# Optimization experiments

Measured on AMD Instinct MI355X. Metric: run time of the kernel, lower is better.

Reference implementation:

```python
import jax, jax.numpy as jnp
import numpy as np

H = 128   # d_model / features
N = 32    # kept complex modes (d_state=64 -> 32 conjugate pairs)
B = 8
L = 8192


def setup_inputs() -> dict:
    key = jax.random.key(0)
    ks = jax.random.split(key, 8)
    x = jax.random.normal(ks[0], (B, H, L), jnp.float32)
    # S4D (diagonal SSM) kernel parameters; channels=2 for bidirectional
    C_re = (jax.random.normal(ks[1], (2, H, N), jnp.float32) * (0.5 ** 0.5))
    C_im = (jax.random.normal(ks[2], (2, H, N), jnp.float32) * (0.5 ** 0.5))
    log_A_real = jnp.log(0.5 * jnp.ones((H, N), jnp.float32))          # S4D-Lin init
    A_imag = jnp.tile(np.pi * jnp.arange(N, dtype=jnp.float32), (H, 1))
    # log_dt uniform in [log(1e-3), log(1e-1)]
    u = jax.random.uniform(ks[3], (H,), jnp.float32)
    log_dt = u * (np.log(0.1) - np.log(0.001)) + np.log(0.001)
    D = jax.random.normal(ks[4], (H,), jnp.float32)                    # skip term
    W_pw = jax.random.normal(ks[5], (H, H), jnp.float32) / np.sqrt(H)  # 1x1 conv weight (out, in)
    gamma = jnp.ones((H,), jnp.float32)
    beta = jnp.zeros((H,), jnp.float32)
    return {"x": x, "C_re": C_re, "C_im": C_im, "log_A_real": log_A_real,
            "A_imag": A_imag, "log_dt": log_dt, "D": D, "W_pw": W_pw,
            "gamma": gamma, "beta": beta}


def reference(x, C_re, C_im, log_A_real, A_imag, log_dt, D, W_pw, gamma, beta):
    Lx = x.shape[-1]
    # ---- S4D SSM kernel via Vandermonde (ZOH discretization) ----
    A = -jnp.exp(log_A_real) + 1j * A_imag                 # (H, N) complex
    dt = jnp.exp(log_dt)[:, None]                          # (H, 1)
    dtA = A * dt                                           # (H, N)
    C = C_re + 1j * C_im                                   # (2, H, N)
    Kc = C * ((jnp.exp(dtA) - 1.0) / A)                    # (2, H, N)
    vand = jnp.exp(dtA[:, :, None] * jnp.arange(Lx))       # (H, N, L)
    k = 2.0 * jnp.einsum('chn,hnl->chl', Kc, vand).real    # (2, H, L)
    # ---- bidirectional: causal half + anticausal (flipped) half ----
    k_full = (jnp.pad(k[0], ((0, 0), (0, Lx)))
              + jnp.pad(k[1][:, ::-1], ((0, 0), (Lx, 0))))  # (H, 2L)
    # ---- FFT convolution ----
    n = 2 * Lx
    y = jnp.fft.irfft(jnp.fft.rfft(x, n=n) * jnp.fft.rfft(k_full, n=n), n=n)[..., :Lx]
    y = y + x * D[:, None]                                 # skip connection
    y = jax.nn.gelu(y, approximate=False)                  # FFTConv default activation
    # ---- pointwise 1x1 conv (no bias) ----
    y = jnp.einsum('bhl,oh->bol', y, W_pw)
    # ---- BatchNorm1d (training-mode batch statistics) ----
    mean = jnp.mean(y, axis=(0, 2), keepdims=True)
    var = jnp.var(y, axis=(0, 2), keepdims=True)
    y = (y - mean) * jax.lax.rsqrt(var + 1e-5) * gamma[:, None] + beta[:, None]
    # ---- ELU + residual (dropout p=0) ----
    return jax.nn.elu(y) + x
```

## Files before the change

kernel.cpp:

```cpp
#include <hip/hip_runtime.h>
#include <math.h>

#define HCH   128
#define NMODE 32
#define BB    8
#define LLEN  8192
#define LC    256
#define CCH   (LLEN / LC)
#define ROWS  (BB * HCH)

typedef unsigned int uint;
typedef _Float16 f16x8 __attribute__((ext_vector_type(8)));
typedef float    f32x4 __attribute__((ext_vector_type(4)));

static __device__ __forceinline__ uint pk2(float a, float b) {
    union { _Float16 h[2]; uint u; } v;
    v.h[0] = (_Float16)a; v.h[1] = (_Float16)b;
    return v.u;
}

__device__ __forceinline__ float gelu_f(float y) {
    float z = fabsf(y) * 0.7071067811865476f;
    float p = fmaf(z, 0.078108f, 0.000972f);
    p = fmaf(z, p, 0.230389f);
    p = fmaf(z, p, 0.278393f);
    p = fmaf(z, p, 1.0f);
    float p2 = p * p;
    float p4 = p2 * p2;
    float er = 1.f - __builtin_amdgcn_rcpf(p4);
    float s  = copysignf(er, y);
    return 0.5f * y * (1.f + s);
}

#define DPP_ADD(v, ctrl) { int _t = __builtin_amdgcn_update_dpp(0, __float_as_int(v), \
                             (ctrl), 0xF, 0xF, true); (v) += __int_as_float(_t); }

__global__ __launch_bounds__(256) void k_prep(const float* __restrict__ C_re,
                                              const float* __restrict__ C_im,
                                              const float* __restrict__ logA,
                                              const float* __restrict__ Aim,
                                              const float* __restrict__ logdt,
                                              const float* __restrict__ W,
                                              _Float16* __restrict__ aT,
                                              _Float16* __restrict__ eT,
                                              _Float16* __restrict__ Wh,
                                              float* __restrict__ Pw,
                                              float* __restrict__ stats) {
    __shared__ float2 PL[32 * 257];
    __shared__ float4 G01[32];
    __shared__ float4 HG[32];
    __shared__ float2 WL[32];
    __shared__ float k0L[256], k1L[256];
    int tid  = threadIdx.x;
    int h    = blockIdx.x >> 1;
    int half = blockIdx.x & 1;
    if (blockIdx.x == 0) stats[tid] = 0.f;
    if (half == 0 && tid < 128) Wh[h * 128 + tid] = (_Float16)W[h * 128 + tid];
    if (tid < 32) {
        int n = tid, idx = h * 32 + n;
        float ar = expf(logA[idx]);
        float ai = Aim[idx];
        float dt = expf(logdt[h]);
        float dre = -ar * dt, dim = ai * dt;
        float er = expf(dre);
        float wr = er * cosf(dim), wi = er * sinf(dim);
        WL[n] = (float2){wr, wi};
        if (half == 0) {
            float eL = expf(dre * 256.f);
            Pw[idx]        = eL * cosf(dim * 256.f);
            Pw[4096 + idx] = eL * sinf(dim * 256.f);
        }
        float den  = ar * ar + ai * ai;
        float numr = -(wr - 1.f) * ar + wi * ai;
        float numi = -wi * ar - (wr - 1.f) * ai;
        float Kr = numr / den, Ki = numi / den;
        float c0r = C_re[idx],        c0i = C_im[idx];
        float c1r = C_re[4096 + idx], c1i = C_im[4096 + idx];
        float g0r = 2.f * (c0r * Kr - c0i * Ki), g0i = 2.f * (c0r * Ki + c0i * Kr);
        float g1r = 2.f * (c1r * Kr - c1i * Ki);
        float g1i = 2.f * (c1r * Ki + c1i * Kr);
        G01[n] = (float4){g0r, g0i, g1r, g1i};
        HG[n]  = (float4){g0r * wr - g0i * wi, g0r * wi + g0i * wr, g1r, g1i};
    }
    __syncthreads();
    {
        int n = tid & 31, tg = tid >> 5;
        float2 w = WL[n];
        float w2r = w.x * w.x - w.y * w.y,   w2i = 2.f * w.x * w.y;
        float w4r = w2r * w2r - w2i * w2i,   w4i = 2.f * w2r * w2i;
        float w8r = w4r * w4r - w4i * w4i,   w8i = 2.f * w4r * w4i;
        float pr = (tg & 1) ? w.x : 1.f;
        float pi = (tg & 1) ? w.y : 0.f;
        if (tg & 2) { float t2 = pr * w2r - pi * w2i; pi = pr * w2i + pi * w2r; pr = t2; }
        if (tg & 4) { float t4 = pr * w4r - pi * w4i; pi = pr * w4i + pi * w4r; pr = t4; }
        float2* row = &PL[n * 257];
        #pragma unroll
        for (int j = 0; j < 32; j++) {
            row[tg + 8 * j] = (float2){pr, pi};
            float tr = pr * w8r - pi * w8i; pi = pr * w8i + pi * w8r; pr = tr;
        }
    }
    __syncthreads();
    {
        int tau = tid;
        float s0 = 0.f, s1 = 0.f;
        #pragma unroll
        for (int n = 0; n < 32; n++) {
            float2 p = PL[n * 257 + tau];
            float4 g = G01[n];
            s0 += g.x * p.x - g.y * p.y;
            s1 += g.z * p.x - g.w * p.y;
        }
        k0L[tau] = s0; k1L[tau] = s1;
    }
    __syncthreads();
    #pragma unroll 4
    for (int i = 0; i < 64; i++) {
        int idx = i * 256 + tid;
        int t  = half * 128 + (idx >> 7);
        int sp = (idx & 127) << 1;
        float v0 = (sp     <= t) ? k0L[t - sp]     : k1L[sp - t - 1];
        float v1 = (sp + 1 <= t) ? k0L[t - sp - 1] : k1L[sp - t];
        *(uint*)&aT[((size_t)(h * 256 + t)) * 384 + sp] = pk2(v0, v1);
    }
    #pragma unroll 4
    for (int i = 0; i < 16; i++) {
        int idx = i * 256 + tid;
        int n = idx & 31;
        int t = half * 128 + (idx >> 5);
        float2 pt = PL[n * 257 + t];
        float2 pu = PL[n * 257 + 255 - t];
        float4 hg = HG[n];
        size_t rb = ((size_t)(h * 256 + t)) * 384;
        *(uint*)&aT[rb + 256 + 2 * n] = pk2(hg.x * pt.x - hg.y * pt.y,
                                            -(hg.x * pt.y + hg.y * pt.x));
        *(uint*)&aT[rb + 320 + 2 * n] = pk2(hg.z * pu.x - hg.w * pu.y,
                                            -(hg.z * pu.y + hg.w * pu.x));
    }
    #pragma unroll 4
    for (int i = 0; i < 16; i++) {
        int idx = i * 256 + tid;
        int n = idx >> 7;
        int s = half * 128 + (idx & 127);
        float2 ps = PL[n * 257 + s];
        float2 pu = PL[n * 257 + 255 - s];
        size_t base = (size_t)h * 128 * 256;
        eT[base + (size_t)(2 * n) * 256 + s]      = (_Float16)pu.x;
        eT[base + (size_t)(2 * n + 1) * 256 + s]  = (_Float16)pu.y;
        eT[base + (size_t)(64 + 2 * n) * 256 + s] = (_Float16)ps.x;
        eT[base + (size_t)(65 + 2 * n) * 256 + s] = (_Float16)ps.y;
    }
}

__global__ __launch_bounds__(256, 2) void k_states_g(const float* __restrict__ x,
                                                     const _Float16* __restrict__ eT,
                                                     float* __restrict__ S_end,
                                                     _Float16* __restrict__ xh) {
    __shared__ _Float16 At[2][128 * 40];
    __shared__ _Float16 Bt[2][128 * 40];
    int tid = threadIdx.x;
    int xcd = blockIdx.x & 7, slot = blockIdx.x >> 3;
    int h = xcd * 16 + (slot >> 1), mt = slot & 1;
    int wave = tid >> 6, lane = tid & 63;
    int wm = wave >> 1, wn = wave & 1;
    int lrow = lane & 15, quad = lane >> 4;
    int koff = quad * 8;
    f32x4 acc[4][4];
    #pragma unroll
    for (int a = 0; a < 4; a++)
        #pragma unroll
        for (int b = 0; b < 4; b++) acc[a][b] = (f32x4){0.f, 0.f, 0.f, 0.f};

    const int chA = tid >> 3, segA = tid & 7;
    const size_t xbase = (((size_t)(mt * 4) * HCH + h) << 13) + (chA << 8) + segA * 4;
    const int rB = tid >> 2, sgB = tid & 3;

    float4 ar[4]; uint4 br[2];
    #define LOADA_S(kk) { _Pragma("unroll") for (int i = 0; i < 4; i++) \
        ar[i] = *(const float4*)(x + xbase + ((size_t)i << 20) + (kk)); }
    #define LOADB_S(kk) { _Pragma("unroll") for (int i = 0; i < 2; i++) \
        br[i] = *(const uint4*)(eT + ((size_t)(h * 128 + rB + 64 * i)) * 256 + (kk) + sgB * 8); }
    #define WRITE_S(buf, kk) { _Pragma("unroll") for (int i = 0; i < 4; i++) { \
            uint2 o; o.x = pk2(ar[i].x, ar[i].y); o.y = pk2(ar[i].z, ar[i].w); \
            *(uint2*)&At[buf][(chA + 32 * i) * 40 + segA * 4] = o; \
            *(uint2*)&xh[xbase + ((size_t)i << 20) + (kk)] = o; } \
        _Pragma("unroll") for (int i = 0; i < 2; i++) \
            *(uint4*)&Bt[buf][(rB + 64 * i) * 40 + sgB * 8] = br[i]; }

    LOADA_S(0); LOADB_S(0);
    WRITE_S(0, 0);
    __syncthreads();
    for (int kt = 0; kt < 8; kt++) {
        int cur = kt & 1;
        if (kt < 7) { LOADA_S((kt + 1) * 32); LOADB_S((kt + 1) * 32); }
        f16x8 a[4], b[4];
        #pragma unroll
        for (int f = 0; f < 4; f++) {
            a[f] = *(const f16x8*)&At[cur][(wm * 64 + f * 16 + lrow) * 40 + koff];
            b[f] = *(const f16x8*)&Bt[cur][(wn * 64 + f * 16 + lrow) * 40 + koff];
        }
        #pragma unroll
        for (int fi = 0; fi < 4; fi++)
            #pragma unroll
            for (int fj = 0; fj < 4; fj++)
                acc[fi][fj] = __builtin_amdgcn_mfma_f32_16x16x32_f16(a[fi], b[fj], acc[fi][fj], 0, 0, 0);
        if (kt < 7) {
            WRITE_S(cur ^ 1, (kt + 1) * 32);
            __syncthreads();
        }
    }
    #pragma unroll
    for (int fi = 0; fi < 4; fi++) {
        #pragma unroll
        for (int fj = 0; fj < 4; fj++) {
            int srow = wn * 64 + fj * 16 + lrow;
            #pragma unroll
            for (int rg = 0; rg < 4; rg++) {
                int bc = mt * 128 + wm * 64 + fi * 16 + quad * 4 + rg;
                S_end[((size_t)(h * 256 + bc)) * 128 + srow] = acc[fi][fj][rg];
            }
        }
    }
    #undef LOADA_S
    #undef LOADB_S
    #undef WRITE_S
}

__global__ void k_carries(const float* __restrict__ S_end, const float* __restrict__ Pw,
                          _Float16* __restrict__ carr) {
    int i = blockIdx.x * 256 + threadIdx.x;
    int n = i & 31; int d = (i >> 5) & 1; int row = i >> 6;
    int h = row & (HCH - 1), b = row >> 7;
    int pi = h * NMODE + n;
    float wLr = Pw[pi], wLi = Pw[4096 + pi];
    int srow = d * 64 + 2 * n;
    float cr = 0.f, ci = 0.f;
    if (d == 0) {
        for (int c = 0; c < CCH; c++) {
            size_t base = ((size_t)(h * 256 + b * 32 + c)) * 128 + srow;
            carr[base] = (_Float16)cr; carr[base + 1] = (_Float16)ci;
            float sr = S_end[base], si = S_end[base + 1];
            float nr = fmaf(wLr, cr, -wLi * ci) + sr;
            float ni = fmaf(wLi, cr,  wLr * ci) + si;
            cr = nr; ci = ni;
        }
    } else {
        for (int c = CCH - 1; c >= 0; c--) {
            size_t base = ((size_t)(h * 256 + b * 32 + c)) * 128 + srow;
            carr[base] = (_Float16)cr; carr[base + 1] = (_Float16)ci;
            float sr = S_end[base], si = S_end[base + 1];
            float nr = fmaf(wLr, cr, -wLi * ci) + sr;
            float ni = fmaf(wLi, cr,  wLr * ci) + si;
            cr = nr; ci = ni;
        }
    }
}

__global__ __launch_bounds__(256, 2) void k_conv_g(const _Float16* __restrict__ xh,
                                                   const _Float16* __restrict__ aT,
                                                   const _Float16* __restrict__ carr,
                                                   const float* __restrict__ D,
                                                   _Float16* __restrict__ Yg) {
    __shared__ _Float16 At[2][128 * 40];
    __shared__ _Float16 Bt[2][128 * 40];
    int tid = threadIdx.x;
    int xcd = blockIdx.x & 7, slot = blockIdx.x >> 3;
    int p = xcd * 32 + (slot >> 1);
    int mt = slot & 1;
    int h = p >> 1, nt = p & 1;
    int wave = tid >> 6, lane = tid & 63;
    int wm = wave >> 1, wn = wave & 1;
    int lrow = lane & 15, quad = lane >> 4;
    int koff = quad * 8;
    f32x4 acc[4][4];
    #pragma unroll
    for (int a = 0; a < 4; a++)
        #pragma unroll
        for (int b = 0; b < 4; b++) acc[a][b] = (f32x4){0.f, 0.f, 0.f, 0.f};

    const int rS = tid >> 2, sgS = tid & 3;

    uint4 a_r[2], b_r[2];
    #define LOADA_C(kk) { _Pragma("unroll") for (int i = 0; i < 2; i++) { \
            int bc = mt * 128 + rS + 64 * i; \
            a_r[i] = ((kk) < 256) \
              ? *(const uint4*)(xh + (((size_t)((bc >> 5) * HCH + h)) << 13) + ((bc & 31) << 8) + (kk) + sgS * 8) \
              : *(const uint4*)(carr + ((size_t)(h * 256 + bc)) * 128 + ((kk) - 256) + sgS * 8); } }
    #define LOADB_C(kk) { _Pragma("unroll") for (int i = 0; i < 2; i++) \
        b_r[i] = *(const uint4*)(aT + ((size_t)(h * 256 + nt * 128 + rS + 64 * i)) * 384 + (kk) + sgS * 8); }
    #define WRITE_C(buf) { _Pragma("unroll") for (int i = 0; i < 2; i++) { \
            *(uint4*)&At[buf][(rS + 64 * i) * 40 + sgS * 8] = a_r[i]; \
            *(uint4*)&Bt[buf][(rS + 64 * i) * 40 + sgS * 8] = b_r[i]; } }

    LOADA_C(0); LOADB_C(0);
    WRITE_C(0);
    __syncthreads();
    for (int kt = 0; kt < 12; kt++) {
        int cur = kt & 1;
        if (kt < 11) { LOADA_C((kt + 1) * 32); LOADB_C((kt + 1) * 32); }
        f16x8 a[4], b[4];
        #pragma unroll
        for (int f = 0; f < 4; f++) {
            a[f] = *(const f16x8*)&At[cur][(wm * 64 + f * 16 + lrow) * 40 + koff];
            b[f] = *(const f16x8*)&Bt[cur][(wn * 64 + f * 16 + lrow) * 40 + koff];
        }
        #pragma unroll
        for (int fi = 0; fi < 4; fi++)
            #pragma unroll
            for (int fj = 0; fj < 4; fj++)
                acc[fi][fj] = __builtin_amdgcn_mfma_f32_16x16x32_f16(a[fi], b[fj], acc[fi][fj], 0, 0, 0);
        if (kt < 11) {
            WRITE_C(cur ^ 1);
            __syncthreads();
        }
    }
    float Dh = D[h];
    #pragma unroll
    for (int fi = 0; fi < 4; fi++) {
        #pragma unroll
        for (int fj = 0; fj < 4; fj++) {
            int t = nt * 128 + wn * 64 + fj * 16 + lrow;
            #pragma unroll
            for (int rg = 0; rg < 4; rg++) {
                int bc = mt * 128 + wm * 64 + fi * 16 + quad * 4 + rg;
                size_t base = (((size_t)((bc >> 5) * HCH + h)) << 13) + ((bc & 31) << 8) + t;
                float xv = (float)xh[base];
                float yv = acc[fi][fj][rg] + Dh * xv;
                Yg[base] = (_Float16)gelu_f(yv);
            }
        }
    }
    #undef LOADA_C
    #undef LOADB_C
    #undef WRITE_C
}

__global__ __launch_bounds__(256, 2) void k_pointwise(const _Float16* __restrict__ Yg,
                                                      const _Float16* __restrict__ Wh,
                                                      _Float16* __restrict__ z,
                                                      float* __restrict__ stats) {
    __shared__ _Float16 Yt[2][128 * 40];
    __shared__ float Ls[512];
    int tid = threadIdx.x;
    int b  = blockIdx.x >> 6;
    int l0 = (blockIdx.x & 63) << 7;
    int wave = tid >> 6, lane = tid & 63;
    int wm = wave >> 1, wn = wave & 1;
    int lrow = lane & 15, quad = lane >> 4;
    int koff = quad * 8;
    f32x4 acc[4][4];
    #pragma unroll
    for (int a = 0; a < 4; a++)
        #pragma unroll
        for (int c = 0; c < 4; c++) acc[a][c] = (f32x4){0.f, 0.f, 0.f, 0.f};

    f16x8 a[4][4];
    #pragma unroll
    for (int ks = 0; ks < 4; ks++)
        #pragma unroll
        for (int f = 0; f < 4; f++)
            a[ks][f] = *(const f16x8*)(Wh + (wm * 64 + f * 16 + lrow) * HCH + ks * 32 + koff);

    const int hhS = tid & 31;
    const int lgbase = tid >> 5;
    uint4 yv[2];
    #define LOADY(kk) { _Pragma("unroll") for (int i = 0; i < 2; i++) \
        yv[i] = *(const uint4*)(Yg + (((size_t)(b * HCH + (kk) + hhS)) << 13) + l0 + (lgbase + 8 * i) * 8); }
    #define WRITEY(buf) { _Pragma("unroll") for (int i = 0; i < 2; i++) { \
            const _Float16* hv = (const _Float16*)&yv[i]; \
            _Pragma("unroll") for (int j = 0; j < 8; j++) \
                Yt[buf][((lgbase + 8 * i) * 8 + j) * 40 + hhS] = hv[j]; } }

    LOADY(0);
    WRITEY(0);
    __syncthreads();
    for (int kt = 0; kt < 4; kt++) {
        int cur = kt & 1;
        if (kt < 3) LOADY((kt + 1) * 32);
        f16x8 bf[4];
        #pragma unroll
        for (int f = 0; f < 4; f++)
            bf[f] = *(const f16x8*)&Yt[cur][(wn * 64 + f * 16 + lrow) * 40 + koff];
        #pragma unroll
        for (int fi = 0; fi < 4; fi++)
            #pragma unroll
            for (int fj = 0; fj < 4; fj++)
                acc[fi][fj] = __builtin_amdgcn_mfma_f32_16x16x32_f16(a[kt][fi], bf[fj], acc[fi][fj], 0, 0, 0);
        if (kt < 3) {
            WRITEY(cur ^ 1);
            __syncthreads();
        }
    }
    #pragma unroll
    for (int fi = 0; fi < 4; fi++) {
        #pragma unroll
        for (int fj = 0; fj < 4; fj++) {
            int l = l0 + wn * 64 + fj * 16 + lrow;
            #pragma unroll
            for (int rg = 0; rg < 4; rg++) {
                int o = wm * 64 + fi * 16 + quad * 4 + rg;
                z[(((size_t)(b * HCH + o)) << 13) + l] = (_Float16)acc[fi][fj][rg];
            }
        }
    }
    #pragma unroll
    for (int fi = 0; fi < 4; fi++) {
        #pragma unroll
        for (int rg = 0; rg < 4; rg++) {
            float s = 0.f, q = 0.f;
            #pragma unroll
            for (int fj = 0; fj < 4; fj++) {
                float v = acc[fi][fj][rg];
                s += v; q = fmaf(v, v, q);
            }
            DPP_ADD(s, 0xB1); DPP_ADD(s, 0x4E); DPP_ADD(s, 0x141); DPP_ADD(s, 0x140);
            DPP_ADD(q, 0xB1); DPP_ADD(q, 0x4E); DPP_ADD(q, 0x141); DPP_ADD(q, 0x140);
            if (lrow == 0) {
                int olo = fi * 16 + quad * 4 + rg;
                Ls[wave * 64 + olo]       = s;
                Ls[256 + wave * 64 + olo] = q;
            }
        }
    }
    __syncthreads();
    if (tid < HCH) {
        int wmn = tid >> 6;
        int olo = tid & 63;
        float s = Ls[(wmn * 2) * 64 + olo] + Ls[(wmn * 2 + 1) * 64 + olo];
        float q = Ls[256 + (wmn * 2) * 64 + olo] + Ls[256 + (wmn * 2 + 1) * 64 + olo];
        atomicAdd(&stats[tid], s);
        atomicAdd(&stats[HCH + tid], q);
    }
    #undef LOADY
    #undef WRITEY
}

__global__ __launch_bounds__(256) void k_final(const _Float16* __restrict__ z,
                                               const float* __restrict__ x,
                                               const float* __restrict__ stats,
                                               const float* __restrict__ gamma,
                                               const float* __restrict__ beta,
                                               float* __restrict__ out) {
    size_t i8 = (size_t)blockIdx.x * 256 + threadIdx.x;
    int o = (int)((i8 >> 10) & (HCH - 1));
    const float inv_cnt = 1.f / (float)(BB * LLEN);
    float m   = stats[o] * inv_cnt;
    float var = stats[HCH + o] * inv_cnt - m * m;
    float rs  = rsqrtf(var + 1e-5f);
    float ga  = gamma[o] * rs;
    float bt  = beta[o] - m * ga;
    uint4 zv = ((const uint4*)z)[i8];
    const _Float16* zh = (const _Float16*)&zv;
    float4 xa = ((const float4*)x)[2 * i8];
    float4 xb = ((const float4*)x)[2 * i8 + 1];
    float4 ra, rb;
    { float t = fmaf((float)zh[0], ga, bt); float e = t > 0.f ? t : (__expf(t) - 1.f); ra.x = e + xa.x; }
    { float t = fmaf((float)zh[1], ga, bt); float e = t > 0.f ? t : (__expf(t) - 1.f); ra.y = e + xa.y; }
    { float t = fmaf((float)zh[2], ga, bt); float e = t > 0.f ? t : (__expf(t) - 1.f); ra.z = e + xa.z; }
    { float t = fmaf((float)zh[3], ga, bt); float e = t > 0.f ? t : (__expf(t) - 1.f); ra.w = e + xa.w; }
    { float t = fmaf((float)zh[4], ga, bt); float e = t > 0.f ? t : (__expf(t) - 1.f); rb.x = e + xb.x; }
    { float t = fmaf((float)zh[5], ga, bt); float e = t > 0.f ? t : (__expf(t) - 1.f); rb.y = e + xb.y; }
    { float t = fmaf((float)zh[6], ga, bt); float e = t > 0.f ? t : (__expf(t) - 1.f); rb.z = e + xb.z; }
    { float t = fmaf((float)zh[7], ga, bt); float e = t > 0.f ? t : (__expf(t) - 1.f); rb.w = e + xb.w; }
    ((float4*)out)[2 * i8]     = ra;
    ((float4*)out)[2 * i8 + 1] = rb;
}

extern "C" void kernel_launch(void* const* d_in, const int* in_sizes, int n_in,
                              void* d_out, int out_size, void* d_ws, size_t ws_size,
                              hipStream_t stream) {
    const float* x     = (const float*)d_in[0];
    const float* C_re  = (const float*)d_in[1];
    const float* C_im  = (const float*)d_in[2];
    const float* logA  = (const float*)d_in[3];
    const float* Aim   = (const float*)d_in[4];
    const float* logdt = (const float*)d_in[5];
    const float* D     = (const float*)d_in[6];
    const float* W     = (const float*)d_in[7];
    const float* gamma = (const float*)d_in[8];
    const float* beta  = (const float*)d_in[9];

    float* ws = (float*)d_ws;
    _Float16* eT    = (_Float16*)ws;
    float*    S_end = ws + 2097152;
    _Float16* Yg    = (_Float16*)ws;
    _Float16* aT    = (_Float16*)(ws + 8388608);
    _Float16* zf    = (_Float16*)(ws + 8388608);
    _Float16* carr  = (_Float16*)(ws + 16777216);
    float*    Pw    = ws + 16777216 + 2097152;
    float*    stats = Pw + 8192;
    _Float16* Wh    = (_Float16*)(ws + 18882816);
    _Float16* xh    = (_Float16*)(ws + 18891008);
    float*    out   = (float*)d_out;

    k_prep     <<<256,  256, 0, stream>>>(C_re, C_im, logA, Aim, logdt, W, aT, eT, Wh, Pw, stats);
    k_states_g <<<256,  256, 0, stream>>>(x, eT, S_end, xh);
    k_carries  <<<256,  256, 0, stream>>>(S_end, Pw, carr);
    k_conv_g   <<<512,  256, 0, stream>>>(xh, aT, carr, D, Yg);
    k_pointwise<<<512,  256, 0, stream>>>(Yg, Wh, zf, stats);
    k_final    <<<4096, 256, 0, stream>>>(zf, x, stats, gamma, beta, out);
}
```

Measured before the change: 182.0 us.

## Fuse carry scan into states kernel and BatchNorm/ELU into pointwise via grid barrier

Moves the chunk-carry recurrence into the states GEMM kernel, using a 64KB shared-memory state tile so S_end no longer round-trips through global memory. It also fuses the final BatchNorm+ELU+residual into the pointwise GEMM kernel with a software grid-wide barrier (an atomic counter spin) after the stats reduction. This removes the fp16 z intermediate and two launches. In exchange, the large shared allocation lowers occupancy of the states kernel, and the spin barrier assumes all 512 blocks are co-resident, risking deadlock if they are not.

```diff
diff --git a/kernel.cpp b/kernel.cpp
--- a/kernel.cpp
+++ b/kernel.cpp
@@ -54,7 +54,10 @@
     int tid  = threadIdx.x;
     int h    = blockIdx.x >> 1;
     int half = blockIdx.x & 1;
-    if (blockIdx.x == 0) stats[tid] = 0.f;
+    if (blockIdx.x == 0) {
+        stats[tid] = 0.f;
+        if (tid == 0) stats[256] = 0.f;
+    }
     if (half == 0 && tid < 128) Wh[h * 128 + tid] = (_Float16)W[h * 128 + tid];
     if (tid < 32) {
         int n = tid, idx = h * 32 + n;
@@ -152,12 +155,14 @@
     }
 }
 
-__global__ __launch_bounds__(256, 2) void k_states_g(const float* __restrict__ x,
-                                                     const _Float16* __restrict__ eT,
-                                                     float* __restrict__ S_end,
-                                                     _Float16* __restrict__ xh) {
+__global__ __launch_bounds__(256) void k_states_c(const float* __restrict__ x,
+                                                  const _Float16* __restrict__ eT,
+                                                  const float* __restrict__ Pw,
+                                                  _Float16* __restrict__ xh,
+                                                  _Float16* __restrict__ carr) {
     __shared__ _Float16 At[2][128 * 40];
     __shared__ _Float16 Bt[2][128 * 40];
+    __shared__ float S[128 * 128];
     int tid = threadIdx.x;
     int xcd = blockIdx.x & 7, slot = blockIdx.x >> 3;
     int h = xcd * 16 + (slot >> 1), mt = slot & 1;
@@ -216,44 +221,43 @@
             int srow = wn * 64 + fj * 16 + lrow;
             #pragma unroll
             for (int rg = 0; rg < 4; rg++) {
-                int bc = mt * 128 + wm * 64 + fi * 16 + quad * 4 + rg;
-                S_end[((size_t)(h * 256 + bc)) * 128 + srow] = acc[fi][fj][rg];
+                int bcl = wm * 64 + fi * 16 + quad * 4 + rg;
+                S[bcl * 128 + srow] = acc[fi][fj][rg];
+            }
+        }
+    }
+    __syncthreads();
+    {
+        int bloc = tid >> 6;
+        int d    = (tid >> 5) & 1;
+        int n    = tid & 31;
+        float wLr = Pw[h * 32 + n], wLi = Pw[4096 + h * 32 + n];
+        int srow = d * 64 + 2 * n;
+        float cr = 0.f, ci = 0.f;
+        size_t gb = ((size_t)(h * 256 + mt * 128 + bloc * 32)) * 128 + srow;
+        if (d == 0) {
+            for (int c = 0; c < CCH; c++) {
+                *(uint*)&carr[gb + (size_t)c * 128] = pk2(cr, ci);
+                float sr = S[(bloc * 32 + c) * 128 + srow];
+                float si = S[(bloc * 32 + c) * 128 + srow + 1];
+                float nr = fmaf(wLr, cr, -wLi * ci) + sr;
+                float ni = fmaf(wLi, cr,  wLr * ci) + si;
+                cr = nr; ci = ni;
+            }
+        } else {
+            for (int c = CCH - 1; c >= 0; c--) {
+                *(uint*)&carr[gb + (size_t)c * 128] = pk2(cr, ci);
+                float sr = S[(bloc * 32 + c) * 128 + srow];
+                float si = S[(bloc * 32 + c) * 128 + srow + 1];
+                float nr = fmaf(wLr, cr, -wLi * ci) + sr;
+                float ni = fmaf(wLi, cr,  wLr * ci) + si;
+                cr = nr; ci = ni;
             }
         }
     }
     #undef LOADA_S
     #undef LOADB_S
     #undef WRITE_S
-}
-
-__global__ void k_carries(const float* __restrict__ S_end, const float* __restrict__ Pw,
-                          _Float16* __restrict__ carr) {
-    int i = blockIdx.x * 256 + threadIdx.x;
-    int n = i & 31; int d = (i >> 5) & 1; int row = i >> 6;
-    int h = row & (HCH - 1), b = row >> 7;
-    int pi = h * NMODE + n;
-    float wLr = Pw[pi], wLi = Pw[4096 + pi];
-    int srow = d * 64 + 2 * n;
-    float cr = 0.f, ci = 0.f;
-    if (d == 0) {
-        for (int c = 0; c < CCH; c++) {
-            size_t base = ((size_t)(h * 256 + b * 32 + c)) * 128 + srow;
-            carr[base] = (_Float16)cr; carr[base + 1] = (_Float16)ci;
-            float sr = S_end[base], si = S_end[base + 1];
-            float nr = fmaf(wLr, cr, -wLi * ci) + sr;
-            float ni = fmaf(wLi, cr,  wLr * ci) + si;
-            cr = nr; ci = ni;
-        }
-    } else {
-        for (int c = CCH - 1; c >= 0; c--) {
-            size_t base = ((size_t)(h * 256 + b * 32 + c)) * 128 + srow;
-            carr[base] = (_Float16)cr; carr[base + 1] = (_Float16)ci;
-            float sr = S_end[base], si = S_end[base + 1];
-            float nr = fmaf(wLr, cr, -wLi * ci) + sr;
-            float ni = fmaf(wLi, cr,  wLr * ci) + si;
-            cr = nr; ci = ni;
-        }
-    }
 }
 
 __global__ __launch_bounds__(256, 2) void k_conv_g(const _Float16* __restrict__ xh,
@@ -335,14 +339,17 @@
     #undef WRITE_C
 }
 
-__global__ __launch_bounds__(256, 2) void k_pointwise(const _Float16* __restrict__ Yg,
-                                                      const _Float16* __restrict__ Wh,
-                                                      _Float16* __restrict__ z,
-                                                      float* __restrict__ stats) {
+__global__ __launch_bounds__(256, 2) void k_pw_final(const _Float16* __restrict__ Yg,
+                                                     const _Float16* __restrict__ Wh,
+                                                     const float* __restrict__ x,
+                                                     const float* __restrict__ gamma,
+                                                     const float* __restrict__ beta,
+                                                     float* __restrict__ stats,
+                                                     float* __restrict__ out) {
     __shared__ _Float16 Yt[2][128 * 40];
     __shared__ float Ls[512];
     int tid = threadIdx.x;
-    int b  = blockIdx.x >> 6;
+    int bb = blockIdx.x >> 6;
     int l0 = (blockIdx.x & 63) << 7;
     int wave = tid >> 6, lane = tid & 63;
     int wm = wave >> 1, wn = wave & 1;
@@ -365,7 +372,7 @@
     const int lgbase = tid >> 5;
     uint4 yv[2];
     #define LOADY(kk) { _Pragma("unroll") for (int i = 0; i < 2; i++) \
-        yv[i] = *(const uint4*)(Yg + (((size_t)(b * HCH + (kk) + hhS)) << 13) + l0 + (lgbase + 8 * i) * 8); }
+        yv[i] = *(const uint4*)(Yg + (((size_t)(bb * HCH + (kk) + hhS)) << 13) + l0 + (lgbase + 8 * i) * 8); }
     #define WRITEY(buf) { _Pragma("unroll") for (int i = 0; i < 2; i++) { \
             const _Float16* hv = (const _Float16*)&yv[i]; \
             _Pragma("unroll") for (int j = 0; j < 8; j++) \
@@ -389,18 +396,6 @@
         if (kt < 3) {
             WRITEY(cur ^ 1);
             __syncthreads();
-        }
-    }
-    #pragma unroll
-    for (int fi = 0; fi < 4; fi++) {
-        #pragma unroll
-        for (int fj = 0; fj < 4; fj++) {
-            int l = l0 + wn * 64 + fj * 16 + lrow;
-            #pragma unroll
-            for (int rg = 0; rg < 4; rg++) {
-                int o = wm * 64 + fi * 16 + quad * 4 + rg;
-                z[(((size_t)(b * HCH + o)) << 13) + l] = (_Float16)acc[fi][fj][rg];
-            }
         }
     }
     #pragma unroll
@@ -431,39 +426,40 @@
         atomicAdd(&stats[tid], s);
         atomicAdd(&stats[HCH + tid], q);
     }
+    __threadfence();
+    __syncthreads();
+    if (tid == 0) {
+        uint* ctr = (uint*)(stats + 256);
+        __hip_atomic_fetch_add(ctr, 1u, __ATOMIC_ACQ_REL, __HIP_MEMORY_SCOPE_AGENT);
+        while (__hip_atomic_load(ctr, __ATOMIC_ACQUIRE, __HIP_MEMORY_SCOPE_AGENT) < 512u)
+            __builtin_amdgcn_s_sleep(2);
+    }
+    __syncthreads();
+    Ls[tid] = __hip_atomic_load(stats + tid, __ATOMIC_RELAXED, __HIP_MEMORY_SCOPE_AGENT);
+    __syncthreads();
+    const float inv_cnt = 1.f / (float)(BB * LLEN);
+    #pragma unroll
+    for (int fi = 0; fi < 4; fi++) {
+        #pragma unroll
+        for (int rg = 0; rg < 4; rg++) {
+            int o = wm * 64 + fi * 16 + quad * 4 + rg;
+            float m   = Ls[o] * inv_cnt;
+            float var = Ls[HCH + o] * inv_cnt - m * m;
+            float rs  = rsqrtf(var + 1e-5f);
+            float ga  = gamma[o] * rs;
+            float bt  = beta[o] - m * ga;
+            size_t rowb = ((size_t)(bb * HCH + o)) << 13;
+            #pragma unroll
+            for (int fj = 0; fj < 4; fj++) {
+                int l = l0 + wn * 64 + fj * 16 + lrow;
+                float t = fmaf(acc[fi][fj][rg], ga, bt);
+                float e = t > 0.f ? t : (__expf(t) - 1.f);
+                out[rowb + l] = e + x[rowb + l];
+            }
+        }
+    }
     #undef LOADY
     #undef WRITEY
-}
-
-__global__ __launch_bounds__(256) void k_final(const _Float16* __restrict__ z,
-                                               const float* __restrict__ x,
-                                               const float* __restrict__ stats,
-                                               const float* __restrict__ gamma,
-                                               const float* __restrict__ beta,
-                                               float* __restrict__ out) {
-    size_t i8 = (size_t)blockIdx.x * 256 + threadIdx.x;
-    int o = (int)((i8 >> 10) & (HCH - 1));
-    const float inv_cnt = 1.f / (float)(BB * LLEN);
-    float m   = stats[o] * inv_cnt;
-    float var = stats[HCH + o] * inv_cnt - m * m;
-    float rs  = rsqrtf(var + 1e-5f);
-    float ga  = gamma[o] * rs;
-    float bt  = beta[o] - m * ga;
-    uint4 zv = ((const uint4*)z)[i8];
-    const _Float16* zh = (const _Float16*)&zv;
-    float4 xa = ((const float4*)x)[2 * i8];
-    float4 xb = ((const float4*)x)[2 * i8 + 1];
-    float4 ra, rb;
-    { float t = fmaf((float)zh[0], ga, bt); float e = t > 0.f ? t : (__expf(t) - 1.f); ra.x = e + xa.x; }
-    { float t = fmaf((float)zh[1], ga, bt); float e = t > 0.f ? t : (__expf(t) - 1.f); ra.y = e + xa.y; }
-    { float t = fmaf((float)zh[2], ga, bt); float e = t > 0.f ? t : (__expf(t) - 1.f); ra.z = e + xa.z; }
-    { float t = fmaf((float)zh[3], ga, bt); float e = t > 0.f ? t : (__expf(t) - 1.f); ra.w = e + xa.w; }
-    { float t = fmaf((float)zh[4], ga, bt); float e = t > 0.f ? t : (__expf(t) - 1.f); rb.x = e + xb.x; }
-    { float t = fmaf((float)zh[5], ga, bt); float e = t > 0.f ? t : (__expf(t) - 1.f); rb.y = e + xb.y; }
-    { float t = fmaf((float)zh[6], ga, bt); float e = t > 0.f ? t : (__expf(t) - 1.f); rb.z = e + xb.z; }
-    { float t = fmaf((float)zh[7], ga, bt); float e = t > 0.f ? t : (__expf(t) - 1.f); rb.w = e + xb.w; }
-    ((float4*)out)[2 * i8]     = ra;
-    ((float4*)out)[2 * i8 + 1] = rb;
 }
 
 extern "C" void kernel_launch(void* const* d_in, const int* in_sizes, int n_in,
@@ -482,21 +478,17 @@
 
     float* ws = (float*)d_ws;
     _Float16* eT    = (_Float16*)ws;
-    float*    S_end = ws + 2097152;
     _Float16* Yg    = (_Float16*)ws;
     _Float16* aT    = (_Float16*)(ws + 8388608);
-    _Float16* zf    = (_Float16*)(ws + 8388608);
     _Float16* carr  = (_Float16*)(ws + 16777216);
     float*    Pw    = ws + 16777216 + 2097152;
     float*    stats = Pw + 8192;
-    _Float16* Wh    = (_Float16*)(ws + 18882816);
-    _Float16* xh    = (_Float16*)(ws + 18891008);
+    _Float16* Wh    = (_Float16*)(ws + 18882880);
+    _Float16* xh    = (_Float16*)(ws + 18891072);
     float*    out   = (float*)d_out;
 
     k_prep     <<<256,  256, 0, stream>>>(C_re, C_im, logA, Aim, logdt, W, aT, eT, Wh, Pw, stats);
-    k_states_g <<<256,  256, 0, stream>>>(x, eT, S_end, xh);
-    k_carries  <<<256,  256, 0, stream>>>(S_end, Pw, carr);
+    k_states_c <<<256,  256, 0, stream>>>(x, eT, Pw, xh, carr);
     k_conv_g   <<<512,  256, 0, stream>>>(xh, aT, carr, D, Yg);
-    k_pointwise<<<512,  256, 0, stream>>>(Yg, Wh, zf, stats);
-    k_final    <<<4096, 256, 0, stream>>>(zf, x, stats, gamma, beta, out);
-}
+    k_pw_final <<<512,  256, 0, stream>>>(Yg, Wh, x, gamma, beta, stats, out);
+}
```

New measurement: 205.9 us. +13.2%, slower.

## Fuse chunk-carry scan into state GEMM kernel via shared memory

Applied to the files above, without the earlier changes.

The separate k_carries kernel is removed. The per-chunk end states are staged in shared memory at the end of k_states_c and the sequential carry recurrence runs there, writing the fp16 carries directly. This avoids the S_end global write and read round-trip and one kernel launch. In exchange, the serial 32-step scan now runs on only 128 threads per block in two passes with extra barriers, which lengthens the tail of the GEMM kernel. Workspace offsets are shifted slightly as a side effect.

```diff
diff --git a/kernel.cpp b/kernel.cpp
--- a/kernel.cpp
+++ b/kernel.cpp
@@ -152,12 +152,12 @@
     }
 }
 
-__global__ __launch_bounds__(256, 2) void k_states_g(const float* __restrict__ x,
+__global__ __launch_bounds__(256, 2) void k_states_c(const float* __restrict__ x,
                                                      const _Float16* __restrict__ eT,
-                                                     float* __restrict__ S_end,
-                                                     _Float16* __restrict__ xh) {
-    __shared__ _Float16 At[2][128 * 40];
-    __shared__ _Float16 Bt[2][128 * 40];
+                                                     const float* __restrict__ Pw,
+                                                     _Float16* __restrict__ xh,
+                                                     _Float16* __restrict__ carr) {
+    __shared__ _Float16 SM[4][5120];
     int tid = threadIdx.x;
     int xcd = blockIdx.x & 7, slot = blockIdx.x >> 3;
     int h = xcd * 16 + (slot >> 1), mt = slot & 1;
@@ -182,10 +182,10 @@
         br[i] = *(const uint4*)(eT + ((size_t)(h * 128 + rB + 64 * i)) * 256 + (kk) + sgB * 8); }
     #define WRITE_S(buf, kk) { _Pragma("unroll") for (int i = 0; i < 4; i++) { \
             uint2 o; o.x = pk2(ar[i].x, ar[i].y); o.y = pk2(ar[i].z, ar[i].w); \
-            *(uint2*)&At[buf][(chA + 32 * i) * 40 + segA * 4] = o; \
+            *(uint2*)&SM[buf][(chA + 32 * i) * 40 + segA * 4] = o; \
             *(uint2*)&xh[xbase + ((size_t)i << 20) + (kk)] = o; } \
         _Pragma("unroll") for (int i = 0; i < 2; i++) \
-            *(uint4*)&Bt[buf][(rB + 64 * i) * 40 + sgB * 8] = br[i]; }
+            *(uint4*)&SM[2 + (buf)][(rB + 64 * i) * 40 + sgB * 8] = br[i]; }
 
     LOADA_S(0); LOADB_S(0);
     WRITE_S(0, 0);
@@ -196,8 +196,8 @@
         f16x8 a[4], b[4];
         #pragma unroll
         for (int f = 0; f < 4; f++) {
-            a[f] = *(const f16x8*)&At[cur][(wm * 64 + f * 16 + lrow) * 40 + koff];
-            b[f] = *(const f16x8*)&Bt[cur][(wn * 64 + f * 16 + lrow) * 40 + koff];
+            a[f] = *(const f16x8*)&SM[cur][(wm * 64 + f * 16 + lrow) * 40 + koff];
+            b[f] = *(const f16x8*)&SM[2 + cur][(wn * 64 + f * 16 + lrow) * 40 + koff];
         }
         #pragma unroll
         for (int fi = 0; fi < 4; fi++)
@@ -209,51 +209,55 @@
             __syncthreads();
         }
     }
-    #pragma unroll
-    for (int fi = 0; fi < 4; fi++) {
-        #pragma unroll
-        for (int fj = 0; fj < 4; fj++) {
-            int srow = wn * 64 + fj * 16 + lrow;
-            #pragma unroll
-            for (int rg = 0; rg < 4; rg++) {
-                int bc = mt * 128 + wm * 64 + fi * 16 + quad * 4 + rg;
-                S_end[((size_t)(h * 256 + bc)) * 128 + srow] = acc[fi][fj][rg];
+    __syncthreads();
+    float* Sf = (float*)SM;
+    #pragma unroll
+    for (int p = 0; p < 2; p++) {
+        if (wm == p) {
+            #pragma unroll
+            for (int fi = 0; fi < 4; fi++) {
+                #pragma unroll
+                for (int fj = 0; fj < 4; fj++) {
+                    int srow = wn * 64 + fj * 16 + lrow;
+                    #pragma unroll
+                    for (int rg = 0; rg < 4; rg++) {
+                        int lb = fi * 16 + quad * 4 + rg;
+                        Sf[lb * 128 + srow] = acc[fi][fj][rg];
+                    }
+                }
             }
         }
+        __syncthreads();
+        if (tid < 128) {
+            int blocL = tid >> 6, d = (tid >> 5) & 1, n = tid & 31;
+            int bloc = p * 2 + blocL;
+            float wLr = Pw[h * 32 + n], wLi = Pw[4096 + h * 32 + n];
+            int srow = d * 64 + 2 * n;
+            float cr = 0.f, ci = 0.f;
+            size_t gb = ((size_t)(h * 256 + mt * 128 + bloc * 32)) * 128 + srow;
+            if (d == 0) {
+                for (int c = 0; c < CCH; c++) {
+                    *(uint*)&carr[gb + (size_t)c * 128] = pk2(cr, ci);
+                    float2 s = *(const float2*)&Sf[(blocL * 32 + c) * 128 + srow];
+                    float nr = fmaf(wLr, cr, -wLi * ci) + s.x;
+                    float ni = fmaf(wLi, cr,  wLr * ci) + s.y;
+                    cr = nr; ci = ni;
+                }
+            } else {
+                for (int c = CCH - 1; c >= 0; c--) {
+                    *(uint*)&carr[gb + (size_t)c * 128] = pk2(cr, ci);
+                    float2 s = *(const float2*)&Sf[(blocL * 32 + c) * 128 + srow];
+                    float nr = fmaf(wLr, cr, -wLi * ci) + s.x;
+                    float ni = fmaf(wLi, cr,  wLr * ci) + s.y;
+                    cr = nr; ci = ni;
+                }
+            }
+        }
+        __syncthreads();
     }
     #undef LOADA_S
     #undef LOADB_S
     #undef WRITE_S
-}
-
-__global__ void k_carries(const float* __restrict__ S_end, const float* __restrict__ Pw,
-                          _Float16* __restrict__ carr) {
-    int i = blockIdx.x * 256 + threadIdx.x;
-    int n = i & 31; int d = (i >> 5) & 1; int row = i >> 6;
-    int h = row & (HCH - 1), b = row >> 7;
-    int pi = h * NMODE + n;
-    float wLr = Pw[pi], wLi = Pw[4096 + pi];
-    int srow = d * 64 + 2 * n;
-    float cr = 0.f, ci = 0.f;
-    if (d == 0) {
-        for (int c = 0; c < CCH; c++) {
-            size_t base = ((size_t)(h * 256 + b * 32 + c)) * 128 + srow;
-            carr[base] = (_Float16)cr; carr[base + 1] = (_Float16)ci;
-            float sr = S_end[base], si = S_end[base + 1];
-            float nr = fmaf(wLr, cr, -wLi * ci) + sr;
-            float ni = fmaf(wLi, cr,  wLr * ci) + si;
-            cr = nr; ci = ni;
-        }
-    } else {
-        for (int c = CCH - 1; c >= 0; c--) {
-            size_t base = ((size_t)(h * 256 + b * 32 + c)) * 128 + srow;
-            carr[base] = (_Float16)cr; carr[base + 1] = (_Float16)ci;
-            float sr = S_end[base], si = S_end[base + 1];
-            float nr = fmaf(wLr, cr, -wLi * ci) + sr;
-            float ni = fmaf(wLi, cr,  wLr * ci) + si;
-            cr = nr; ci = ni;
-        }
-    }
 }
 
 __global__ __launch_bounds__(256, 2) void k_conv_g(const _Float16* __restrict__ xh,
@@ -482,20 +486,18 @@
 
     float* ws = (float*)d_ws;
     _Float16* eT    = (_Float16*)ws;
-    float*    S_end = ws + 2097152;
     _Float16* Yg    = (_Float16*)ws;
     _Float16* aT    = (_Float16*)(ws + 8388608);
     _Float16* zf    = (_Float16*)(ws + 8388608);
     _Float16* carr  = (_Float16*)(ws + 16777216);
     float*    Pw    = ws + 16777216 + 2097152;
     float*    stats = Pw + 8192;
-    _Float16* Wh    = (_Float16*)(ws + 18882816);
-    _Float16* xh    = (_Float16*)(ws + 18891008);
+    _Float16* Wh    = (_Float16*)(ws + 18882880);
+    _Float16* xh    = (_Float16*)(ws + 18891072);
     float*    out   = (float*)d_out;
 
     k_prep     <<<256,  256, 0, stream>>>(C_re, C_im, logA, Aim, logdt, W, aT, eT, Wh, Pw, stats);
-    k_states_g <<<256,  256, 0, stream>>>(x, eT, S_end, xh);
-    k_carries  <<<256,  256, 0, stream>>>(S_end, Pw, carr);
+    k_states_c <<<256,  256, 0, stream>>>(x, eT, Pw, xh, carr);
     k_conv_g   <<<512,  256, 0, stream>>>(xh, aT, carr, D, Yg);
     k_pointwise<<<512,  256, 0, stream>>>(Yg, Wh, zf, stats);
     k_final    <<<4096, 256, 0, stream>>>(zf, x, stats, gamma, beta, out);
```

After: 175.5 us. 3.6% less time.
